# Optimization experiments

Hardware: AMD Instinct MI355X
Metric: run time of the kernel (lower is better)

Reference implementation:

```python
import jax, jax.numpy as jnp
import numpy as np

B, S, HID = 1, 2048, 2048
H, KV, D = 32, 8, 64          # num_heads, num_kv_heads, head_dim
N_REP = H // KV               # GQA groups = 4
FF = 8192
EPS = 1e-5
ROPE_THETA = 10000.0


def _rope_tables(seq_len, dim, dtype=jnp.float32):
    inv_freq = 1.0 / (ROPE_THETA ** (jnp.arange(0, dim, 2, dtype=jnp.float32) / dim))
    t = jnp.arange(seq_len, dtype=jnp.float32)
    freqs = jnp.outer(t, inv_freq)                 # [S, D/2]
    emb = jnp.concatenate([freqs, freqs], axis=-1) # [S, D]
    return jnp.cos(emb).astype(dtype)[None], jnp.sin(emb).astype(dtype)[None]  # [1,S,D]


def setup_inputs() -> dict:
    key = jax.random.key(0)
    ks = jax.random.split(key, 10)
    s = 0.02
    cos, sin = _rope_tables(S, D)
    return {
        "hidden_states": jax.random.normal(ks[0], (B, S, HID), jnp.float32),
        "cos": cos, "sin": sin,
        "wq": jax.random.normal(ks[1], (HID, H * D), jnp.float32) * s,
        "wk": jax.random.normal(ks[2], (HID, KV * D), jnp.float32) * s,
        "wv": jax.random.normal(ks[3], (HID, KV * D), jnp.float32) * s,
        "wo": jax.random.normal(ks[4], (H * D, HID), jnp.float32) * s,
        "w_ln1": jnp.ones((HID,), jnp.float32),
        "w_ln2": jnp.ones((HID,), jnp.float32),
        "w_gate": jax.random.normal(ks[5], (HID, FF), jnp.float32) * s,
        "w_up": jax.random.normal(ks[6], (HID, FF), jnp.float32) * s,
        "w_down": jax.random.normal(ks[7], (FF, HID), jnp.float32) * s,
    }


def _rmsnorm(x, w):
    var = jnp.mean(jnp.square(x), axis=-1, keepdims=True)
    return x * jax.lax.rsqrt(var + EPS) * w


def _rotate_half(x):
    x1, x2 = jnp.split(x, 2, axis=-1)
    return jnp.concatenate([-x2, x1], axis=-1)


def _apply_rope(q, k, cos, sin):
    # q,k: [B,H,S,D]; cos,sin: [B,S,D] -> unsqueeze head dim
    c, s = cos[:, None], sin[:, None]
    return q * c + _rotate_half(q) * s, k * c + _rotate_half(k) * s


def reference(hidden_states, cos, sin, wq, wk, wv, wo, w_ln1, w_ln2, w_gate, w_up, w_down):
    residual = hidden_states
    x = _rmsnorm(hidden_states, w_ln1)

    q = (x @ wq).reshape(B, S, H, D).transpose(0, 2, 1, 3)    # [B,H,S,D]
    k = (x @ wk).reshape(B, S, KV, D).transpose(0, 2, 1, 3)   # [B,KV,S,D]
    v = (x @ wv).reshape(B, S, KV, D).transpose(0, 2, 1, 3)
    q, k = _apply_rope(q, k, cos, sin)

    # repeat_kv (interleaved) for GQA
    k = jnp.repeat(k, N_REP, axis=1)                           # [B,H,S,D]
    v = jnp.repeat(v, N_REP, axis=1)

    scale = 1.0 / np.sqrt(D)
    scores = jnp.einsum("bhqd,bhkd->bhqk", q, k) * scale       # [B,H,S,S]
    causal = jnp.tril(jnp.ones((S, S), bool))
    scores = jnp.where(causal, scores, jnp.finfo(scores.dtype).min)
    probs = jax.nn.softmax(scores, axis=-1)
    attn = jnp.einsum("bhqk,bhkd->bhqd", probs, v)             # [B,H,S,D]
    attn = attn.transpose(0, 2, 1, 3).reshape(B, S, H * D)
    attn = attn @ wo

    h = residual + attn
    residual = h
    y = _rmsnorm(h, w_ln2)
    mlp = (jax.nn.silu(y @ w_gate) * (y @ w_up)) @ w_down
    return residual + mlp
```

## Files before the change

kernel.cpp:

```cpp
#include <hip/hip_runtime.h>
#include <hip/hip_bf16.h>
#include <cstdint>

#define S_LEN 2048
#define HIDN  2048
#define NH    32
#define NKV   8
#define HD    64
#define FFN   8192
#define QKVN  3072
#define QKVLD 3072

typedef __attribute__((ext_vector_type(4)))  float f32x4;
typedef __attribute__((ext_vector_type(16))) float f32x16;
typedef __attribute__((ext_vector_type(8)))  short short8;
typedef __attribute__((ext_vector_type(4)))  short s16x4;

__device__ __forceinline__ short f2bf(float f) {
  union { float f; uint32_t u; } v; v.f = f;
  uint32_t r = v.u + 0x7FFFu + ((v.u >> 16) & 1u);
  return (short)(r >> 16);
}
__device__ __forceinline__ float bf2f(short s) {
  union { float f; uint32_t u; } v; v.u = ((uint32_t)(uint16_t)s) << 16;
  return v.f;
}
__device__ __forceinline__ unsigned packbf2(float lo, float hi) {
  return (unsigned)(uint16_t)f2bf(lo) | ((unsigned)(uint16_t)f2bf(hi) << 16);
}

#define GLOAD_LDS16(gp, lp) \
  __builtin_amdgcn_global_load_lds((const __attribute__((address_space(1))) void*)(gp), \
                                   (__attribute__((address_space(3))) void*)(lp), 16, 0, 0)

#define BARRIER()  asm volatile("s_barrier" ::: "memory")
#define LGKM0()    asm volatile("s_waitcnt lgkmcnt(0)" ::: "memory")
#define SCHED0()   __builtin_amdgcn_sched_barrier(0)
#define VMCNT(N)   asm volatile("s_waitcnt vmcnt(%0)" :: "n"(N) : "memory")

__global__ __launch_bounds__(256) void convT_kernel(const float* __restrict__ src,
    short* __restrict__ dst, int K, int N) {
  __shared__ float t[64][65];
  const int k0 = blockIdx.x * 64, n0 = blockIdx.y * 64;
  const int tr = threadIdx.x >> 4, tc = (threadIdx.x & 15) * 4;
  #pragma unroll
  for (int i = 0; i < 4; ++i) {
    float4 v = *(const float4*)(src + (size_t)(k0 + tr + i * 16) * N + n0 + tc);
    t[tr + i * 16][tc] = v.x; t[tr + i * 16][tc + 1] = v.y;
    t[tr + i * 16][tc + 2] = v.z; t[tr + i * 16][tc + 3] = v.w;
  }
  __syncthreads();
  const int dr = threadIdx.x >> 2, dc = (threadIdx.x & 3) * 16;
  short8 o0, o1;
  #pragma unroll
  for (int j = 0; j < 8; ++j) { o0[j] = f2bf(t[dc + j][dr]); o1[j] = f2bf(t[dc + 8 + j][dr]); }
  short* dp = dst + (size_t)(n0 + dr) * K + k0 + dc;
  *(short8*)dp = o0;
  *(short8*)(dp + 8) = o1;
}

__global__ __launch_bounds__(256) void convT_pack_kernel(const float* __restrict__ src,
    short* __restrict__ dst, int plane) {
  __shared__ float t[64][65];
  const int k0 = blockIdx.x * 64, n0 = blockIdx.y * 64;
  const int tr = threadIdx.x >> 4, tc = (threadIdx.x & 15) * 4;
  #pragma unroll
  for (int i = 0; i < 4; ++i) {
    float4 v = *(const float4*)(src + (size_t)(k0 + tr + i * 16) * FFN + n0 + tc);
    t[tr + i * 16][tc] = v.x; t[tr + i * 16][tc + 1] = v.y;
    t[tr + i * 16][tc + 2] = v.z; t[tr + i * 16][tc + 3] = v.w;
  }
  __syncthreads();
  const int dr = threadIdx.x >> 2, dc = (threadIdx.x & 3) * 16;
  const int n = n0 + dr;
  const int rr = ((n >> 4) << 5) + plane * 16 + (n & 15);
  short8 o0, o1;
  #pragma unroll
  for (int j = 0; j < 8; ++j) { o0[j] = f2bf(t[dc + j][dr]); o1[j] = f2bf(t[dc + 8 + j][dr]); }
  short* dp = dst + (size_t)rr * HIDN + k0 + dc;
  *(short8*)dp = o0;
  *(short8*)(dp + 8) = o1;
}

__global__ __launch_bounds__(256) void rmsnorm_kernel(const float* __restrict__ X,
    const float* __restrict__ W, short* __restrict__ Y) {
  int row = blockIdx.x;
  const float4* x4 = (const float4*)(X + (size_t)row * HIDN);
  const float4* w4 = (const float4*)W;
  float4 v0 = x4[2 * threadIdx.x];
  float4 v1 = x4[2 * threadIdx.x + 1];
  float ss = v0.x*v0.x + v0.y*v0.y + v0.z*v0.z + v0.w*v0.w
           + v1.x*v1.x + v1.y*v1.y + v1.z*v1.z + v1.w*v1.w;
  #pragma unroll
  for (int off = 32; off > 0; off >>= 1) ss += __shfl_xor(ss, off, 64);
  __shared__ float red[4];
  if ((threadIdx.x & 63) == 0) red[threadIdx.x >> 6] = ss;
  __syncthreads();
  ss = red[0] + red[1] + red[2] + red[3];
  float rs = rsqrtf(ss * (1.0f / HIDN) + 1e-5f);
  float4 w0 = w4[2 * threadIdx.x], w1 = w4[2 * threadIdx.x + 1];
  short8 o;
  o[0] = f2bf(v0.x * rs * w0.x); o[1] = f2bf(v0.y * rs * w0.y);
  o[2] = f2bf(v0.z * rs * w0.z); o[3] = f2bf(v0.w * rs * w0.w);
  o[4] = f2bf(v1.x * rs * w1.x); o[5] = f2bf(v1.y * rs * w1.y);
  o[6] = f2bf(v1.z * rs * w1.z); o[7] = f2bf(v1.w * rs * w1.w);
  *(short8*)(Y + (size_t)row * HIDN + threadIdx.x * 8) = o;
}

template<int EPI, int BN>
__global__ __launch_bounds__(512, 1) void gemm8p(const short* __restrict__ A,
    const short* __restrict__ BT, void* __restrict__ Cp, const void* __restrict__ Xp,
    int N, int Kfull, int KC, int gy) {
  constexpr int NFN = BN / 64;
  constexpr int LB  = BN / 128;
  constexpr int VN  = 2 + 2 * LB;
  __shared__ __align__(16) short As[2][256 * 64];
  __shared__ __align__(16) short Bs[2][BN * 64];
  const int tid = threadIdx.x, lane = tid & 63, w = tid >> 6;
  const int wm2 = w >> 2;
  const int wn = (w & 3) * (BN / 4);
  const int l15 = lane & 15, lg = lane >> 4;
  const int cpx = gy >> 3;
  const int xcd = blockIdx.x & 7, cid = blockIdx.x >> 3;
  const int by = xcd * cpx + cid % cpx, bx = cid / cpx;
  const int brow = bx * 256, bcol = by * BN;
  const size_t kbase = (size_t)blockIdx.z * KC;
  const int r8 = lane >> 3, c8 = lane & 7;
  const int gblk = c8 ^ r8;
  const int nt = KC / 64;
  f32x4 acc[8][NFN] = {};
  short8 af[4], bf[2][NFN];

  auto STA = [&](int p, int kt, int h) {
    const size_t kc = kbase + (size_t)kt * 64 + gblk * 8;
    #pragma unroll
    for (int j = 0; j < 2; ++j) {
      const short* g = A + (size_t)(brow + h * 128 + j * 64 + w * 8 + r8) * Kfull + kc;
      GLOAD_LDS16(g, &As[p][(h * 128 + j * 64 + w * 8) * 64]);
    }
  };
  auto STB = [&](int p, int kt, int h) {
    const size_t kc = kbase + (size_t)kt * 64 + gblk * 8;
    #pragma unroll
    for (int j = 0; j < LB; ++j) {
      const short* g = BT + (size_t)(bcol + h * (BN / 2) + j * 64 + w * 8 + r8) * Kfull + kc;
      GLOAD_LDS16(g, &Bs[p][(h * (BN / 2) + j * 64 + w * 8) * 64]);
    }
  };
  auto LDA = [&](int p, int mh, int kk) {
    #pragma unroll
    for (int m = 0; m < 4; ++m) {
      const int row = mh * 128 + wm2 * 64 + m * 16 + l15;
      af[m] = *(const short8*)&As[p][row * 64 + (((kk * 4 + lg) ^ (row & 7)) * 8)];
    }
  };
  auto LDB = [&](int p, int kk) {
    #pragma unroll
    for (int n = 0; n < NFN; ++n) {
      const int row = wn + n * 16 + l15;
      bf[kk][n] = *(const short8*)&Bs[p][row * 64 + (((kk * 4 + lg) ^ (row & 7)) * 8)];
    }
  };

#define MMQ(MH, KK) \
  __builtin_amdgcn_s_setprio(1); \
  _Pragma("unroll") \
  for (int m = 0; m < 4; ++m) \
    _Pragma("unroll") \
    for (int n = 0; n < NFN; ++n) \
      acc[(MH) * 4 + m][n] = __builtin_amdgcn_mfma_f32_16x16x32_bf16(af[m], bf[KK][n], acc[(MH) * 4 + m][n], 0, 0, 0); \
  __builtin_amdgcn_s_setprio(0);

  STB(0, 0, 0); STB(0, 0, 1); STA(0, 0, 0); STA(0, 0, 1);
  STB(1, 1, 0); STB(1, 1, 1); STA(1, 1, 0);
  VMCNT(VN);
  BARRIER();

  for (int i = 0; i < nt / 2; ++i) {
    const int t = 2 * i;
    const bool li = (i == nt / 2 - 1);
    LDA(0, 0, 0); LDB(0, 0); LDB(0, 1);
    STA(1, t + 1, 1);
    BARRIER(); LGKM0(); SCHED0();
    MMQ(0, 0);
    BARRIER();
    LDA(0, 0, 1);
    if (!li) STB(0, t + 2, 0);
    BARRIER(); LGKM0(); SCHED0();
    MMQ(0, 1);
    BARRIER();
    LDA(0, 1, 0);
    if (!li) STB(0, t + 2, 1);
    BARRIER(); LGKM0(); SCHED0();
    MMQ(1, 0);
    BARRIER();
    LDA(0, 1, 1);
    if (!li) STA(0, t + 2, 0);
    BARRIER(); LGKM0(); SCHED0();
    MMQ(1, 1);
    if (li) { VMCNT(0); } else { VMCNT(VN); }
    BARRIER();
    LDA(1, 0, 0); LDB(1, 0); LDB(1, 1);
    if (!li) STA(0, t + 2, 1);
    BARRIER(); LGKM0(); SCHED0();
    MMQ(0, 0);
    BARRIER();
    LDA(1, 0, 1);
    if (!li) STB(1, t + 3, 0);
    BARRIER(); LGKM0(); SCHED0();
    MMQ(0, 1);
    BARRIER();
    LDA(1, 1, 0);
    if (!li) STB(1, t + 3, 1);
    BARRIER(); LGKM0(); SCHED0();
    MMQ(1, 0);
    BARRIER();
    LDA(1, 1, 1);
    if (!li) STA(1, t + 3, 0);
    BARRIER(); LGKM0(); SCHED0();
    MMQ(1, 1);
    if (!li) { VMCNT(VN); }
    BARRIER();
  }
#undef MMQ

  if (EPI == 4) {
    const int No = N >> 1;
    #pragma unroll
    for (int mf = 0; mf < 8; ++mf) {
      const int r0 = brow + (mf >> 2) * 128 + wm2 * 64 + (mf & 3) * 16 + lg * 4;
      #pragma unroll
      for (int jg = 0; jg < NFN / 2; ++jg) {
        const int c = (bcol >> 1) + (wn >> 1) + jg * 16 + l15;
        #pragma unroll
        for (int i4 = 0; i4 < 4; ++i4) {
          float gt = acc[mf][2 * jg][i4];
          float up = acc[mf][2 * jg + 1][i4];
          ((short*)Cp)[(size_t)(r0 + i4) * No + c] = f2bf(gt / (1.f + __expf(-gt)) * up);
        }
      }
    }
  } else {
    #pragma unroll
    for (int mf = 0; mf < 8; ++mf) {
      const int r0 = brow + (mf >> 2) * 128 + wm2 * 64 + (mf & 3) * 16 + lg * 4;
      #pragma unroll
      for (int nf = 0; nf < NFN; ++nf) {
        const int c = bcol + wn + nf * 16 + l15;
        #pragma unroll
        for (int i4 = 0; i4 < 4; ++i4) {
          const size_t idx = (size_t)(r0 + i4) * N + c;
          float v = acc[mf][nf][i4];
          if (EPI == 0) ((short*)Cp)[idx] = f2bf(v);
          if (EPI == 2) {
            float gf = bf2f(((const short*)Xp)[idx]);
            ((short*)Cp)[idx] = f2bf(gf / (1.f + __expf(-gf)) * v);
          }
          if (EPI == 3) ((float*)Cp)[(size_t)blockIdx.z * S_LEN * N + idx] = v;
        }
      }
    }
  }
}

template<int EPI>
__global__ __launch_bounds__(256) void gemm_bt(const short* __restrict__ A,
    const short* __restrict__ BT, void* __restrict__ Cp, const void* __restrict__ Xp,
    int M, int N, int Kfull, int KC, int gx) {
  __shared__ __align__(16) short Ass[128 * 64];
  __shared__ __align__(16) short Bss[128 * 64];
  const int tid = threadIdx.x, lane = tid & 63, w = tid >> 6;
  const int wm = (w >> 1) * 64, wn = (w & 1) * 64;
  const int l15 = lane & 15, lg = lane >> 4;
  const int nwg = gridDim.x;
  const int qq = nwg >> 3, xcd = blockIdx.x & 7, off = blockIdx.x >> 3;
  const int wg = xcd * qq + off;
  const int brow = (wg % gx) * 128, bcol = (wg / gx) * 128;
  const size_t kbase = (size_t)blockIdx.y * KC;
  const int srow8 = lane >> 3;
  const int gblk  = (lane & 7) ^ (srow8 & 7);
  f32x4 acc[4][4] = {};

  for (int k0 = 0; k0 < KC; k0 += 64) {
    #pragma unroll
    for (int j = 0; j < 4; ++j) {
      const int rbase = w * 32 + j * 8;
      const int row = rbase + srow8;
      const short* ga = A + (size_t)(brow + row) * Kfull + kbase + k0 + gblk * 8;
      GLOAD_LDS16(ga, Ass + rbase * 64);
      const short* gb = BT + (size_t)(bcol + row) * Kfull + kbase + k0 + gblk * 8;
      GLOAD_LDS16(gb, Bss + rbase * 64);
    }
    __syncthreads();
    #pragma unroll
    for (int kk = 0; kk < 2; ++kk) {
      short8 af[4], bf[4];
      #pragma unroll
      for (int m = 0; m < 4; ++m) {
        const int row = wm + m * 16 + l15;
        af[m] = *(const short8*)&Ass[row * 64 + (((kk * 4 + lg) ^ (l15 & 7)) * 8)];
      }
      #pragma unroll
      for (int n = 0; n < 4; ++n) {
        const int row = wn + n * 16 + l15;
        bf[n] = *(const short8*)&Bss[row * 64 + (((kk * 4 + lg) ^ (l15 & 7)) * 8)];
      }
      #pragma unroll
      for (int m = 0; m < 4; ++m)
        #pragma unroll
        for (int n = 0; n < 4; ++n)
          acc[m][n] = __builtin_amdgcn_mfma_f32_16x16x32_bf16(af[m], bf[n], acc[m][n], 0, 0, 0);
    }
    __syncthreads();
  }

  const int r0 = brow + wm + lg * 4;
  const int c0 = bcol + wn + l15;
  #pragma unroll
  for (int m = 0; m < 4; ++m)
    #pragma unroll
    for (int n = 0; n < 4; ++n)
      #pragma unroll
      for (int i = 0; i < 4; ++i) {
        const size_t idx = (size_t)(r0 + m * 16 + i) * N + (c0 + n * 16);
        float v = acc[m][n][i];
        if (EPI == 0) ((short*)Cp)[idx] = f2bf(v);
        if (EPI == 1) ((float*)Cp)[idx] = v + ((const float*)Xp)[idx];
        if (EPI == 2) {
          float gf = bf2f(((const short*)Xp)[idx]);
          ((short*)Cp)[idx] = f2bf(gf / (1.f + __expf(-gf)) * v);
        }
        if (EPI == 3) ((float*)Cp)[(size_t)blockIdx.y * M * N + idx] = v;
      }
}

__global__ __launch_bounds__(256) void rope_kernel(short* __restrict__ qkv,
    const float* __restrict__ cosb, const float* __restrict__ sinb) {
  int idx = blockIdx.x * 256 + threadIdx.x;
  int d = idx & 31;
  int hh = (idx >> 5) % (NH + NKV);
  int s = idx / (32 * (NH + NKV));
  int col = (hh < NH) ? hh * HD : HIDN + (hh - NH) * HD;
  short* base = qkv + (size_t)s * QKVLD + col;
  float c  = cosb[s * HD + d];
  float sn = sinb[s * HD + d];
  float x1 = bf2f(base[d]), x2 = bf2f(base[d + 32]);
  base[d]      = f2bf(x1 * c - x2 * sn);
  base[d + 32] = f2bf(x2 * c + x1 * sn);
}

__global__ __launch_bounds__(256) void attn_kernel(const short* __restrict__ QKV,
    short* __restrict__ O) {
  __shared__ __align__(16) short Ks[64][72];
  __shared__ __align__(16) short VTs[64][72];
  const int bid = blockIdx.x;
  const int half = bid >> 8, idx = bid & 255;
  const int h = idx & 31;
  int qt = idx >> 5;
  qt = half ? (15 - qt) : qt;
  const int kvh = h >> 2;
  const int tid = threadIdx.x, lane = tid & 63, w = tid >> 6;
  const int l31 = lane & 31, hi = lane >> 5;
  const int qb = qt * 128 + w * 32;
  const int kcol = HIDN + kvh * HD;
  const int vcol = HIDN + NKV * HD + kvh * HD;

  short8 Qr[4];
  {
    const short* qp = QKV + (size_t)(qb + l31) * QKVLD + h * HD;
    #pragma unroll
    for (int dk = 0; dk < 4; ++dk) {
      short8 qv = *(const short8*)(qp + dk * 16 + hi * 8);
      #pragma unroll
      for (int e = 0; e < 8; ++e) Qr[dk][e] = f2bf(bf2f(qv[e]) * 0.125f);
    }
  }
  float m_ = -3e38f, l_ = 0.f;
  f32x16 o0 = {}, o1 = {};
  const int nt = 2 * qt + 2;
  const int krow = tid >> 2, kcb = (tid & 3) * 16;
  const int vk = tid & 31, vdb = (tid >> 5) * 8;

  short8 kr0, kr1, vr0, vr1;
  {
    const short* gk = QKV + (size_t)krow * QKVLD + kcol + kcb;
    kr0 = *(const short8*)gk; kr1 = *(const short8*)(gk + 8);
    vr0 = *(const short8*)(QKV + (size_t)vk * QKVLD + vcol + vdb);
    vr1 = *(const short8*)(QKV + (size_t)(32 + vk) * QKVLD + vcol + vdb);
  }

  for (int t = 0; t < nt; ++t) {
    const int kb = t * 64;
    BARRIER();
    *(short8*)&Ks[krow][kcb] = kr0;
    *(short8*)&Ks[krow][kcb + 8] = kr1;
    #pragma unroll
    for (int j = 0; j < 8; ++j) VTs[vdb + j][vk] = vr0[j];
    #pragma unroll
    for (int j = 0; j < 8; ++j) VTs[vdb + j][32 + vk] = vr1[j];
    LGKM0();
    BARRIER();
    if (t + 1 < nt) {
      const int kb2 = kb + 64;
      const short* gk = QKV + (size_t)(kb2 + krow) * QKVLD + kcol + kcb;
      kr0 = *(const short8*)gk; kr1 = *(const short8*)(gk + 8);
      vr0 = *(const short8*)(QKV + (size_t)(kb2 + vk) * QKVLD + vcol + vdb);
      vr1 = *(const short8*)(QKV + (size_t)(kb2 + 32 + vk) * QKVLD + vcol + vdb);
    }
    if (kb < qb + 32) {
      f32x16 s[2] = {};
      __builtin_amdgcn_s_setprio(1);
      #pragma unroll
      for (int kt = 0; kt < 2; ++kt)
        #pragma unroll
        for (int dk = 0; dk < 4; ++dk) {
          short8 kf = *(const short8*)&Ks[kt * 32 + l31][dk * 16 + hi * 8];
          s[kt] = __builtin_amdgcn_mfma_f32_32x32x16_bf16(kf, Qr[dk], s[kt], 0, 0, 0);
        }
      __builtin_amdgcn_s_setprio(0);
      if (kb + 63 > qb) {
        const int qg = qb + l31;
        #pragma unroll
        for (int kt = 0; kt < 2; ++kt)
          #pragma unroll
          for (int r = 0; r < 16; ++r) {
            const int kg = kb + kt * 32 + (r & 3) + 8 * (r >> 2) + 4 * hi;
            if (kg > qg) s[kt][r] = -1e30f;
          }
      }
      float pm = s[0][0];
      #pragma unroll
      for (int r = 1; r < 16; ++r) pm = fmaxf(pm, s[0][r]);
      #pragma unroll
      for (int r = 0; r < 16; ++r) pm = fmaxf(pm, s[1][r]);
      pm = fmaxf(pm, __shfl_xor(pm, 32));
      const float mn = fmaxf(m_, pm);
      const float al = __expf(m_ - mn);
      float rsum = 0.f;
      #pragma unroll
      for (int kt = 0; kt < 2; ++kt)
        #pragma unroll
        for (int r = 0; r < 16; ++r) { s[kt][r] = __expf(s[kt][r] - mn); rsum += s[kt][r]; }
      rsum += __shfl_xor(rsum, 32);
      l_ = l_ * al + rsum;
      m_ = mn;
      o0 *= al; o1 *= al;
      unsigned wd[2][8], rw[2][8];
      #pragma unroll
      for (int kt = 0; kt < 2; ++kt)
        #pragma unroll
        for (int i = 0; i < 8; ++i) {
          wd[kt][i] = packbf2(s[kt][2 * i], s[kt][2 * i + 1]);
          rw[kt][i] = (unsigned)__shfl_xor((int)wd[kt][i], 32);
        }
      #pragma unroll
      for (int kt = 0; kt < 2; ++kt) {
        union { unsigned u[4]; short8 s8; } pf0, pf1;
        if (hi) {
          pf0.u[0] = rw[kt][2]; pf0.u[1] = rw[kt][3]; pf0.u[2] = wd[kt][2]; pf0.u[3] = wd[kt][3];
          pf1.u[0] = rw[kt][6]; pf1.u[1] = rw[kt][7]; pf1.u[2] = wd[kt][6]; pf1.u[3] = wd[kt][7];
        } else {
          pf0.u[0] = wd[kt][0]; pf0.u[1] = wd[kt][1]; pf0.u[2] = rw[kt][0]; pf0.u[3] = rw[kt][1];
          pf1.u[0] = wd[kt][4]; pf1.u[1] = wd[kt][5]; pf1.u[2] = rw[kt][4]; pf1.u[3] = rw[kt][5];
        }
        __builtin_amdgcn_s_setprio(1);
        #pragma unroll
        for (int ks = 0; ks < 2; ++ks) {
          const short8 pB = ks ? pf1.s8 : pf0.s8;
          short8 va = *(const short8*)&VTs[l31][kt * 32 + ks * 16 + hi * 8];
          o0 = __builtin_amdgcn_mfma_f32_32x32x16_bf16(va, pB, o0, 0, 0, 0);
          short8 vb = *(const short8*)&VTs[32 + l31][kt * 32 + ks * 16 + hi * 8];
          o1 = __builtin_amdgcn_mfma_f32_32x32x16_bf16(vb, pB, o1, 0, 0, 0);
        }
        __builtin_amdgcn_s_setprio(0);
      }
    }
  }
  const float inv = 1.f / l_;
  short* op = O + (size_t)(qb + l31) * HIDN + h * HD;
  #pragma unroll
  for (int dt = 0; dt < 2; ++dt) {
    const f32x16& o = dt ? o1 : o0;
    #pragma unroll
    for (int g = 0; g < 4; ++g) {
      s16x4 st;
      st[0] = f2bf(o[g * 4 + 0] * inv);
      st[1] = f2bf(o[g * 4 + 1] * inv);
      st[2] = f2bf(o[g * 4 + 2] * inv);
      st[3] = f2bf(o[g * 4 + 3] * inv);
      *(s16x4*)(op + dt * 32 + g * 8 + hi * 4) = st;
    }
  }
}

__global__ __launch_bounds__(256) void reduce_kernel(float* __restrict__ out,
    const float* __restrict__ P) {
  const size_t n = (size_t)S_LEN * HIDN;
  size_t i = ((size_t)blockIdx.x * 256 + threadIdx.x) * 4;
  float4 o = *(float4*)(out + i);
  float4 a = *(const float4*)(P + i);
  float4 b = *(const float4*)(P + n + i);
  o.x += a.x + b.x; o.y += a.y + b.y; o.z += a.z + b.z; o.w += a.w + b.w;
  *(float4*)(out + i) = o;
}

extern "C" void kernel_launch(void* const* d_in, const int* in_sizes, int n_in,
                              void* d_out, int out_size, void* d_ws, size_t ws_size,
                              hipStream_t stream) {
  const float* hs   = (const float*)d_in[0];
  const float* cosb = (const float*)d_in[1];
  const float* sinb = (const float*)d_in[2];
  const float* wq   = (const float*)d_in[3];
  const float* wk   = (const float*)d_in[4];
  const float* wv   = (const float*)d_in[5];
  const float* wo   = (const float*)d_in[6];
  const float* wln1 = (const float*)d_in[7];
  const float* wln2 = (const float*)d_in[8];
  const float* wg   = (const float*)d_in[9];
  const float* wu   = (const float*)d_in[10];
  const float* wd   = (const float*)d_in[11];
  float* out = (float*)d_out;
  char* ws = (char*)d_ws;
  const size_t MB = 1024 * 1024;
  short* Wbig  = (short*)(ws);
  short* Wqkv  = Wbig;
  short* xn    = (short*)(ws + 13 * MB);
  short* qkv   = (short*)(ws + 21 * MB);
  short* attnO = (short*)(ws + 34 * MB);
  short* Wwo   = (short*)(ws + 42 * MB);
  short* y     = (short*)(ws + 64 * MB);
  short* g     = (short*)(ws + 72 * MB);
  short* Wd    = Wbig;
  float* P     = (float*)(ws + 32 * MB);

  convT_kernel<<<dim3(32, 32), 256, 0, stream>>>(wq, Wqkv, HIDN, NH * HD);
  convT_kernel<<<dim3(32, 8),  256, 0, stream>>>(wk, Wqkv + (size_t)2048 * HIDN, HIDN, NKV * HD);
  convT_kernel<<<dim3(32, 8),  256, 0, stream>>>(wv, Wqkv + (size_t)2560 * HIDN, HIDN, NKV * HD);
  rmsnorm_kernel<<<S_LEN, 256, 0, stream>>>(hs, wln1, xn);
  gemm8p<0, 128><<<dim3(192, 1, 1), 512, 0, stream>>>(xn, Wqkv, qkv, nullptr, QKVN, HIDN, HIDN, 24);
  convT_kernel<<<dim3(32, 32), 256, 0, stream>>>(wo, Wwo, NH * HD, HIDN);
  rope_kernel<<<(S_LEN * (NH + NKV) * 32) / 256, 256, 0, stream>>>(qkv, cosb, sinb);
  attn_kernel<<<NH * (S_LEN / 128), 256, 0, stream>>>(qkv, attnO);
  gemm_bt<1><<<dim3(16 * 16, 1), 256, 0, stream>>>(attnO, Wwo, out, hs, S_LEN, HIDN, NH * HD, NH * HD, 16);
  rmsnorm_kernel<<<S_LEN, 256, 0, stream>>>(out, wln2, y);
  convT_pack_kernel<<<dim3(32, 128), 256, 0, stream>>>(wg, Wbig, 0);
  convT_pack_kernel<<<dim3(32, 128), 256, 0, stream>>>(wu, Wbig, 1);
  gemm8p<4, 256><<<dim3(512, 1, 1), 512, 0, stream>>>(y, Wbig, g, nullptr, 2 * FFN, HIDN, HIDN, 64);
  convT_kernel<<<dim3(128, 32), 256, 0, stream>>>(wd, Wd, FFN, HIDN);
  gemm8p<3, 128><<<dim3(128, 1, 2), 512, 0, stream>>>(g, Wd, P, nullptr, HIDN, FFN, FFN / 2, 16);
  reduce_kernel<<<(S_LEN * HIDN) / 1024, 256, 0, stream>>>(out, P);
}
```

Baseline: 438.6 us.

## Use gemm8p for O-proj, bf16 split-K partials, fused packing, packed SwiGLU stores

Replaces the simple gemm_bt O-projection with the pipelined gemm8p kernel plus a residual epilogue. Changes the down-projection to a 4-way split-K with 256-wide tiles writing bf16 partials, summed by a new reduce kernel. Merges the gate and up weight packing into one launch, and makes the SwiGLU epilogue store two bf16 values per lane via a shuffle. Rounding the split-K partials to bf16 costs some accuracy, and wider tiles leave fewer workgroups.

```diff
diff --git a/kernel.cpp b/kernel.cpp
--- a/kernel.cpp
+++ b/kernel.cpp
@@ -59,9 +59,11 @@
   *(short8*)(dp + 8) = o1;
 }
 
-__global__ __launch_bounds__(256) void convT_pack_kernel(const float* __restrict__ src,
-    short* __restrict__ dst, int plane) {
+__global__ __launch_bounds__(256) void convT_pack2_kernel(const float* __restrict__ wg,
+    const float* __restrict__ wu, short* __restrict__ dst) {
   __shared__ float t[64][65];
+  const int plane = blockIdx.z;
+  const float* src = plane ? wu : wg;
   const int k0 = blockIdx.x * 64, n0 = blockIdx.y * 64;
   const int tr = threadIdx.x >> 4, tc = (threadIdx.x & 15) * 4;
   #pragma unroll
@@ -226,6 +228,7 @@
 
   if (EPI == 4) {
     const int No = N >> 1;
+    const bool evn = (l15 & 1) == 0;
     #pragma unroll
     for (int mf = 0; mf < 8; ++mf) {
       const int r0 = brow + (mf >> 2) * 128 + wm2 * 64 + (mf & 3) * 16 + lg * 4;
@@ -236,7 +239,10 @@
         for (int i4 = 0; i4 < 4; ++i4) {
           float gt = acc[mf][2 * jg][i4];
           float up = acc[mf][2 * jg + 1][i4];
-          ((short*)Cp)[(size_t)(r0 + i4) * No + c] = f2bf(gt / (1.f + __expf(-gt)) * up);
+          float r = gt / (1.f + __expf(-gt)) * up;
+          float ro = __shfl_xor(r, 1);
+          if (evn)
+            *(unsigned*)((short*)Cp + (size_t)(r0 + i4) * No + c) = packbf2(r, ro);
         }
       }
     }
@@ -252,86 +258,12 @@
           const size_t idx = (size_t)(r0 + i4) * N + c;
           float v = acc[mf][nf][i4];
           if (EPI == 0) ((short*)Cp)[idx] = f2bf(v);
-          if (EPI == 2) {
-            float gf = bf2f(((const short*)Xp)[idx]);
-            ((short*)Cp)[idx] = f2bf(gf / (1.f + __expf(-gf)) * v);
-          }
-          if (EPI == 3) ((float*)Cp)[(size_t)blockIdx.z * S_LEN * N + idx] = v;
+          if (EPI == 1) ((float*)Cp)[idx] = v + ((const float*)Xp)[idx];
+          if (EPI == 5) ((short*)Cp)[(size_t)blockIdx.z * S_LEN * N + idx] = f2bf(v);
         }
       }
     }
   }
-}
-
-template<int EPI>
-__global__ __launch_bounds__(256) void gemm_bt(const short* __restrict__ A,
-    const short* __restrict__ BT, void* __restrict__ Cp, const void* __restrict__ Xp,
-    int M, int N, int Kfull, int KC, int gx) {
-  __shared__ __align__(16) short Ass[128 * 64];
-  __shared__ __align__(16) short Bss[128 * 64];
-  const int tid = threadIdx.x, lane = tid & 63, w = tid >> 6;
-  const int wm = (w >> 1) * 64, wn = (w & 1) * 64;
-  const int l15 = lane & 15, lg = lane >> 4;
-  const int nwg = gridDim.x;
-  const int qq = nwg >> 3, xcd = blockIdx.x & 7, off = blockIdx.x >> 3;
-  const int wg = xcd * qq + off;
-  const int brow = (wg % gx) * 128, bcol = (wg / gx) * 128;
-  const size_t kbase = (size_t)blockIdx.y * KC;
-  const int srow8 = lane >> 3;
-  const int gblk  = (lane & 7) ^ (srow8 & 7);
-  f32x4 acc[4][4] = {};
-
-  for (int k0 = 0; k0 < KC; k0 += 64) {
-    #pragma unroll
-    for (int j = 0; j < 4; ++j) {
-      const int rbase = w * 32 + j * 8;
-      const int row = rbase + srow8;
-      const short* ga = A + (size_t)(brow + row) * Kfull + kbase + k0 + gblk * 8;
-      GLOAD_LDS16(ga, Ass + rbase * 64);
-      const short* gb = BT + (size_t)(bcol + row) * Kfull + kbase + k0 + gblk * 8;
-      GLOAD_LDS16(gb, Bss + rbase * 64);
-    }
-    __syncthreads();
-    #pragma unroll
-    for (int kk = 0; kk < 2; ++kk) {
-      short8 af[4], bf[4];
-      #pragma unroll
-      for (int m = 0; m < 4; ++m) {
-        const int row = wm + m * 16 + l15;
-        af[m] = *(const short8*)&Ass[row * 64 + (((kk * 4 + lg) ^ (l15 & 7)) * 8)];
-      }
-      #pragma unroll
-      for (int n = 0; n < 4; ++n) {
-        const int row = wn + n * 16 + l15;
-        bf[n] = *(const short8*)&Bss[row * 64 + (((kk * 4 + lg) ^ (l15 & 7)) * 8)];
-      }
-      #pragma unroll
-      for (int m = 0; m < 4; ++m)
-        #pragma unroll
-        for (int n = 0; n < 4; ++n)
-          acc[m][n] = __builtin_amdgcn_mfma_f32_16x16x32_bf16(af[m], bf[n], acc[m][n], 0, 0, 0);
-    }
-    __syncthreads();
-  }
-
-  const int r0 = brow + wm + lg * 4;
-  const int c0 = bcol + wn + l15;
-  #pragma unroll
-  for (int m = 0; m < 4; ++m)
-    #pragma unroll
-    for (int n = 0; n < 4; ++n)
-      #pragma unroll
-      for (int i = 0; i < 4; ++i) {
-        const size_t idx = (size_t)(r0 + m * 16 + i) * N + (c0 + n * 16);
-        float v = acc[m][n][i];
-        if (EPI == 0) ((short*)Cp)[idx] = f2bf(v);
-        if (EPI == 1) ((float*)Cp)[idx] = v + ((const float*)Xp)[idx];
-        if (EPI == 2) {
-          float gf = bf2f(((const short*)Xp)[idx]);
-          ((short*)Cp)[idx] = f2bf(gf / (1.f + __expf(-gf)) * v);
-        }
-        if (EPI == 3) ((float*)Cp)[(size_t)blockIdx.y * M * N + idx] = v;
-      }
 }
 
 __global__ __launch_bounds__(256) void rope_kernel(short* __restrict__ qkv,
@@ -493,14 +425,18 @@
   }
 }
 
-__global__ __launch_bounds__(256) void reduce_kernel(float* __restrict__ out,
-    const float* __restrict__ P) {
+__global__ __launch_bounds__(256) void reduce4_kernel(float* __restrict__ out,
+    const short* __restrict__ P) {
   const size_t n = (size_t)S_LEN * HIDN;
   size_t i = ((size_t)blockIdx.x * 256 + threadIdx.x) * 4;
   float4 o = *(float4*)(out + i);
-  float4 a = *(const float4*)(P + i);
-  float4 b = *(const float4*)(P + n + i);
-  o.x += a.x + b.x; o.y += a.y + b.y; o.z += a.z + b.z; o.w += a.w + b.w;
+  float s0 = 0.f, s1 = 0.f, s2 = 0.f, s3 = 0.f;
+  #pragma unroll
+  for (int z = 0; z < 4; ++z) {
+    s16x4 p = *(const s16x4*)(P + z * n + i);
+    s0 += bf2f(p[0]); s1 += bf2f(p[1]); s2 += bf2f(p[2]); s3 += bf2f(p[3]);
+  }
+  o.x += s0; o.y += s1; o.z += s2; o.w += s3;
   *(float4*)(out + i) = o;
 }
 
@@ -531,7 +467,7 @@
   short* y     = (short*)(ws + 64 * MB);
   short* g     = (short*)(ws + 72 * MB);
   short* Wd    = Wbig;
-  float* P     = (float*)(ws + 32 * MB);
+  short* P     = (short*)(ws + 32 * MB);
 
   convT_kernel<<<dim3(32, 32), 256, 0, stream>>>(wq, Wqkv, HIDN, NH * HD);
   convT_kernel<<<dim3(32, 8),  256, 0, stream>>>(wk, Wqkv + (size_t)2048 * HIDN, HIDN, NKV * HD);
@@ -541,12 +477,11 @@
   convT_kernel<<<dim3(32, 32), 256, 0, stream>>>(wo, Wwo, NH * HD, HIDN);
   rope_kernel<<<(S_LEN * (NH + NKV) * 32) / 256, 256, 0, stream>>>(qkv, cosb, sinb);
   attn_kernel<<<NH * (S_LEN / 128), 256, 0, stream>>>(qkv, attnO);
-  gemm_bt<1><<<dim3(16 * 16, 1), 256, 0, stream>>>(attnO, Wwo, out, hs, S_LEN, HIDN, NH * HD, NH * HD, 16);
+  gemm8p<1, 128><<<dim3(128, 1, 1), 512, 0, stream>>>(attnO, Wwo, out, hs, HIDN, NH * HD, NH * HD, 16);
   rmsnorm_kernel<<<S_LEN, 256, 0, stream>>>(out, wln2, y);
-  convT_pack_kernel<<<dim3(32, 128), 256, 0, stream>>>(wg, Wbig, 0);
-  convT_pack_kernel<<<dim3(32, 128), 256, 0, stream>>>(wu, Wbig, 1);
+  convT_pack2_kernel<<<dim3(32, 128, 2), 256, 0, stream>>>(wg, wu, Wbig);
   gemm8p<4, 256><<<dim3(512, 1, 1), 512, 0, stream>>>(y, Wbig, g, nullptr, 2 * FFN, HIDN, HIDN, 64);
   convT_kernel<<<dim3(128, 32), 256, 0, stream>>>(wd, Wd, FFN, HIDN);
-  gemm8p<3, 128><<<dim3(128, 1, 2), 512, 0, stream>>>(g, Wd, P, nullptr, HIDN, FFN, FFN / 2, 16);
-  reduce_kernel<<<(S_LEN * HIDN) / 1024, 256, 0, stream>>>(out, P);
-}
+  gemm8p<5, 256><<<dim3(64, 1, 4), 512, 0, stream>>>(g, Wd, P, nullptr, HIDN, FFN, FFN / 4, 8);
+  reduce4_kernel<<<(S_LEN * HIDN) / 1024, 256, 0, stream>>>(out, P);
+}
```

Result: no change. 434.1 us (-1.0%).
